# Kernel optimization log

Measured on AMD Instinct MI355X. Metric: run time of the kernel, lower is better.

## Reference

```python
import jax, jax.numpy as jnp
import numpy as np

H = 768        # bert hidden_size
HID = 512      # lstm_hidden
HALF = HID // 2
T = 20         # tagset_size
START, STOP = 18, 19
S = 16386      # input positions incl. CLS/SEP
NEG = -10000.0


def setup_inputs() -> dict:
    key = jax.random.key(0)
    ks = jax.random.split(key, 12)
    sc_x = 1.0
    x = jax.random.normal(ks[0], (1, S, H), dtype=jnp.float32)
    # PyTorch LSTM params (gate order i,f,g,o), one layer, bidirectional
    s_ih = 1.0 / np.sqrt(HALF)
    w_ih_f = jax.random.uniform(ks[1], (4 * HALF, H), jnp.float32, -s_ih, s_ih)
    w_hh_f = jax.random.uniform(ks[2], (4 * HALF, HALF), jnp.float32, -s_ih, s_ih)
    b_ih_f = jax.random.uniform(ks[3], (4 * HALF,), jnp.float32, -s_ih, s_ih)
    b_hh_f = jax.random.uniform(ks[4], (4 * HALF,), jnp.float32, -s_ih, s_ih)
    w_ih_b = jax.random.uniform(ks[5], (4 * HALF, H), jnp.float32, -s_ih, s_ih)
    w_hh_b = jax.random.uniform(ks[6], (4 * HALF, HALF), jnp.float32, -s_ih, s_ih)
    b_ih_b = jax.random.uniform(ks[7], (4 * HALF,), jnp.float32, -s_ih, s_ih)
    b_hh_b = jax.random.uniform(ks[8], (4 * HALF,), jnp.float32, -s_ih, s_ih)
    s_t = 1.0 / np.sqrt(HID)
    w_tag = jax.random.uniform(ks[9], (T, HID), jnp.float32, -s_t, s_t)
    b_tag = jax.random.uniform(ks[10], (T,), jnp.float32, -s_t, s_t)
    transitions = jax.random.normal(ks[11], (T, T), dtype=jnp.float32)
    transitions = transitions.at[START, :].set(NEG).at[:, STOP].set(NEG)
    return {
        "x": x,
        "w_ih_f": w_ih_f, "w_hh_f": w_hh_f, "b_ih_f": b_ih_f, "b_hh_f": b_hh_f,
        "w_ih_b": w_ih_b, "w_hh_b": w_hh_b, "b_ih_b": b_ih_b, "b_hh_b": b_hh_b,
        "w_tag": w_tag, "b_tag": b_tag, "transitions": transitions,
    }


def _lstm_one_step(xt, w_ih, b_ih, b_hh):
    # Original passes [1, N, H] to a batch_first=False LSTM => seq_len=1,
    # batch=N, zero initial state. So each token does ONE cell step:
    # h0=c0=0 => hh contribution is only b_hh.
    g = xt @ w_ih.T + b_ih + b_hh          # [N, 4*HALF]
    i, f, gg, o = jnp.split(g, 4, axis=-1)  # PyTorch gate order i,f,g,o
    c = jax.nn.sigmoid(i) * jnp.tanh(gg)    # f*c0 = 0
    return jax.nn.sigmoid(o) * jnp.tanh(c)  # [N, HALF]


def reference(x, w_ih_f, w_hh_f, b_ih_f, b_hh_f,
              w_ih_b, w_hh_b, b_ih_b, b_hh_b,
              w_tag, b_tag, transitions):
    tok = x[0, 1:-1, :]                     # narrow(1,1,S-2): drop CLS/SEP -> [N,H]
    h_f = _lstm_one_step(tok, w_ih_f, b_ih_f, b_hh_f)
    h_b = _lstm_one_step(tok, w_ih_b, b_ih_b, b_hh_b)
    enc = jnp.concatenate([h_f, h_b], axis=-1)   # [N, HID]
    feats = enc @ w_tag.T + b_tag                # [N, T] emission scores

    # ---- Viterbi decode (sequential DP over tokens) ----
    init = jnp.full((T,), NEG, dtype=feats.dtype).at[START].set(0.0)

    def vstep(fv, feat):
        scores = fv[None, :] + transitions       # [next_tag, prev_tag]
        bp = jnp.argmax(scores, axis=1)          # backpointers [T]
        fv_new = jnp.max(scores, axis=1) + feat
        return fv_new, bp

    fv, bps = jax.lax.scan(vstep, init, feats)   # bps: [N, T]
    terminal = fv + transitions[STOP]
    best = jnp.argmax(terminal)
    path_score = terminal[best]

    def btrack(b, bp):
        return bp[b], b                          # emit tag at time t, move to t-1

    _, best_path = jax.lax.scan(btrack, best, bps, reverse=True)  # [N] in time order
    return path_score, best_path
```

## Files before the change

### kernel.cpp

```cpp
#include <hip/hip_runtime.h>
#include <math.h>

#define HDIM 768
#define HIDD 512
#define NTOK 16384
#define NT 20
#define CHUNKS 128
#define CLEN 128

typedef unsigned short ushort_t;
typedef __attribute__((ext_vector_type(8))) short bf16x8;
typedef __attribute__((ext_vector_type(4))) float f32x4;

__device__ __forceinline__ float sigm(float x){ return 1.0f/(1.0f+expf(-x)); }

__device__ __forceinline__ ushort_t f2bf(float f){
    unsigned int u = __float_as_uint(f);
    unsigned int r = (u + 0x7fffu + ((u >> 16) & 1u)) >> 16;
    return (ushort_t)r;
}
__device__ __forceinline__ float bf2f(ushort_t b){
    return __uint_as_float(((unsigned int)b) << 16);
}

#define GLD16(gp, lp) __builtin_amdgcn_global_load_lds( \
    (const __attribute__((address_space(1))) void*)(gp), \
    (__attribute__((address_space(3))) void*)(lp), 16, 0, 0)

union U8 { ushort_t u[8]; uint4 v; };

__global__ __launch_bounds__(256) void conv_kernel(
    const float* __restrict__ wf, const float* __restrict__ wb,
    ushort_t* __restrict__ Bh, ushort_t* __restrict__ Bl)
{
    int t = blockIdx.x*256 + threadIdx.x;
    int n = t / 192, c4 = (t - n*192)*4;
    int dir = n / 768, nr = n - dir*768;
    int gate = nr >> 8, j = nr & 255;
    int wrow = j + ((gate==0)?0:((gate==1)?512:768));
    const float* src = dir ? wb : wf;
    const float4 v = *(const float4*)(src + (size_t)wrow*HDIM + c4);
    float f[4] = {v.x, v.y, v.z, v.w};
    ushort_t h[4], l[4];
    #pragma unroll
    for (int i=0;i<4;++i){
        h[i] = f2bf(f[i]);
        l[i] = f2bf(f[i] - bf2f(h[i]));
    }
    *(ushort4*)(Bh + (size_t)n*HDIM + c4) = make_ushort4(h[0],h[1],h[2],h[3]);
    *(ushort4*)(Bl + (size_t)n*HDIM + c4) = make_ushort4(l[0],l[1],l[2],l[3]);
}

__global__ __launch_bounds__(256, 2) void gemm_fused(
    const float* __restrict__ x,
    const ushort_t* __restrict__ Bh, const ushort_t* __restrict__ Bl,
    const float* __restrict__ bihf, const float* __restrict__ bhhf,
    const float* __restrict__ bihb, const float* __restrict__ bhhb,
    const float* __restrict__ wtag, float* __restrict__ featsp)
{
    __shared__ __align__(16) char smem[40960];
    ushort_t* As_h = (ushort_t*)smem;
    ushort_t* As_l = (ushort_t*)(smem + 4096);
    float* hbuf = (float*)smem;
    float* wts  = (float*)(smem + 16512);

    const int tid = threadIdx.x;
    const int bx = blockIdx.x;
    const int xcd = bx & 7, bidx = bx >> 3;
    const int q = bidx & 3, mt = (bidx >> 2)*8 + xcd;
    const int dir = q >> 1, j0 = (q & 1)*128;
    const int row0 = mt*64;
    const float* __restrict__ bih = dir ? bihb : bihf;
    const float* __restrict__ bhh = dir ? bhhb : bhhf;

    const int lane = tid & 63, wv = tid >> 6;
    const int wm = wv >> 1, wn = wv & 1;
    const int lm = lane & 15, lq = lane >> 4;
    const int wb8 = (tid & 192) * 8;

    const int P_ = tid >> 3, s_ = tid & 7;
    const int q_ = s_ ^ (P_ & 7);
    const int mA = (P_ << 1) | (q_ >> 2);
    const int k8s = q_ & 3;
    const int nB  = mA;
    const float* aSrc = x + (size_t)(row0 + mA + 1)*HDIM + k8s*8;
    const int bOff = nB*HDIM + k8s*8;

    int aoff[2], boff[4];
    #pragma unroll
    for (int f=0; f<2; ++f){
        int m = wm*32 + f*16 + lm;
        aoff[f] = ((m>>1)*8 + ((((m&1)<<2)|lq) ^ ((m>>1)&7)))*8;
    }
    #pragma unroll
    for (int f=0; f<4; ++f){
        int n = wn*64 + f*16 + lm;
        boff[f] = ((n>>1)*8 + ((((n&1)<<2)|lq) ^ ((n>>1)&7)))*8;
    }

    int jcol[4];
    #pragma unroll
    for (int fn=0; fn<4; ++fn) jcol[fn] = j0 + wn*64 + fn*16 + lm;

    float held[2][4][4];
    f32x4 acc[2][4];
    uint4 rh, rl;

    {
        const size_t bb = (size_t)(dir*768 + j0)*HDIM;
        GLD16(Bh + bb + bOff,            smem + 8192  + wb8*2);
        GLD16(Bh + bb + bOff + 64*HDIM,  smem + 12288 + wb8*2);
        GLD16(Bl + bb + bOff,            smem + 16384 + wb8*2);
        GLD16(Bl + bb + bOff + 64*HDIM,  smem + 20480 + wb8*2);
        float4 ra0 = *(const float4*)(aSrc);
        float4 ra1 = *(const float4*)(aSrc + 4);
        float f[8] = {ra0.x,ra0.y,ra0.z,ra0.w,ra1.x,ra1.y,ra1.z,ra1.w};
        U8 h8, l8;
        #pragma unroll
        for (int i=0;i<8;++i){
            ushort_t h = f2bf(f[i]);
            h8.u[i] = h; l8.u[i] = f2bf(f[i] - bf2f(h));
        }
        rh = h8.v; rl = l8.v;
    }

    #pragma unroll 1
    for (int p=0; p<3; ++p){
        #pragma unroll
        for (int fm=0; fm<2; ++fm)
            #pragma unroll
            for (int fn=0; fn<4; ++fn)
                acc[fm][fn] = (f32x4){0.f,0.f,0.f,0.f};

        #pragma unroll 1
        for (int kt=0; kt<24; ++kt){
            __syncthreads();
            *(uint4*)&As_h[tid*8] = rh;
            *(uint4*)&As_l[tid*8] = rl;
            __syncthreads();

            int nkt = kt + 1, np = p;
            if (nkt == 24){ nkt = 0; ++np; }
            if (np < 3){
                const int k0n = nkt*32;
                const size_t bb = (size_t)(dir*768 + np*256 + j0)*HDIM + k0n;
                char* bh_d = smem + 8192 + (nkt&1)*16384;
                GLD16(Bh + bb + bOff,           bh_d + wb8*2);
                GLD16(Bh + bb + bOff + 64*HDIM, bh_d + 4096 + wb8*2);
                GLD16(Bl + bb + bOff,           bh_d + 8192 + wb8*2);
                GLD16(Bl + bb + bOff + 64*HDIM, bh_d + 12288 + wb8*2);
                float4 ra0 = *(const float4*)(aSrc + k0n);
                float4 ra1 = *(const float4*)(aSrc + k0n + 4);
                float f[8] = {ra0.x,ra0.y,ra0.z,ra0.w,ra1.x,ra1.y,ra1.z,ra1.w};
                U8 h8, l8;
                #pragma unroll
                for (int i=0;i<8;++i){
                    ushort_t h = f2bf(f[i]);
                    h8.u[i] = h; l8.u[i] = f2bf(f[i] - bf2f(h));
                }
                rh = h8.v; rl = l8.v;
            }

            const ushort_t* Bsh = (const ushort_t*)(smem + 8192 + (kt&1)*16384);
            const ushort_t* Bsl = (const ushort_t*)(smem + 16384 + (kt&1)*16384);
            bf16x8 afh[2], afl[2];
            #pragma unroll
            for (int f=0; f<2; ++f){
                afh[f] = *(const bf16x8*)&As_h[aoff[f]];
                afl[f] = *(const bf16x8*)&As_l[aoff[f]];
            }
            #pragma unroll
            for (int fn=0; fn<4; ++fn){
                bf16x8 bh = *(const bf16x8*)&Bsh[boff[fn]];
                bf16x8 bl = *(const bf16x8*)&Bsl[boff[fn]];
                #pragma unroll
                for (int fm=0; fm<2; ++fm){
                    acc[fm][fn] = __builtin_amdgcn_mfma_f32_16x16x32_bf16(
                        afh[fm], bh, acc[fm][fn], 0, 0, 0);
                    acc[fm][fn] = __builtin_amdgcn_mfma_f32_16x16x32_bf16(
                        afl[fm], bh, acc[fm][fn], 0, 0, 0);
                    acc[fm][fn] = __builtin_amdgcn_mfma_f32_16x16x32_bf16(
                        afh[fm], bl, acc[fm][fn], 0, 0, 0);
                }
            }
        }

        const int gbase = (p==0) ? 0 : ((p==1) ? 512 : 768);
        float bias[4];
        #pragma unroll
        for (int fn=0; fn<4; ++fn)
            bias[fn] = bih[gbase + jcol[fn]] + bhh[gbase + jcol[fn]];

        if (p==0){
            #pragma unroll
            for (int fm=0; fm<2; ++fm)
                #pragma unroll
                for (int fn=0; fn<4; ++fn)
                    #pragma unroll
                    for (int r=0; r<4; ++r)
                        held[fm][fn][r] = sigm(acc[fm][fn][r] + bias[fn]);
        } else if (p==1){
            #pragma unroll
            for (int fm=0; fm<2; ++fm)
                #pragma unroll
                for (int fn=0; fn<4; ++fn)
                    #pragma unroll
                    for (int r=0; r<4; ++r)
                        held[fm][fn][r] *= tanhf(acc[fm][fn][r] + bias[fn]);
        } else {
            float hv[2][4][4];
            #pragma unroll
            for (int fm=0; fm<2; ++fm)
                #pragma unroll
                for (int fn=0; fn<4; ++fn)
                    #pragma unroll
                    for (int r=0; r<4; ++r)
                        hv[fm][fn][r] = sigm(acc[fm][fn][r] + bias[fn]) * tanhf(held[fm][fn][r]);

            __syncthreads();
            for (int i2=tid; i2<NT*128; i2+=256){
                int t = i2 >> 7, j = i2 & 127;
                wts[i2] = wtag[t*HIDD + dir*256 + j0 + j];
            }
            float* fq = featsp + (size_t)q * (NTOK*NT);
            #pragma unroll 1
            for (int ph=0; ph<2; ++ph){
                __syncthreads();
                if (wm == ph){
                    #pragma unroll
                    for (int fm=0; fm<2; ++fm)
                        #pragma unroll
                        for (int fn=0; fn<4; ++fn)
                            #pragma unroll
                            for (int r=0; r<4; ++r){
                                int mloc = fm*16 + lq*4 + r;
                                int jloc = wn*64 + fn*16 + lm;
                                hbuf[mloc*129 + jloc] = hv[fm][fn][r];
                            }
                }
                __syncthreads();
                const int mrow = tid & 31, grp = tid >> 5;
                if (grp < 5){
                    const int tg0 = grp*4;
                    float s[4] = {0.f,0.f,0.f,0.f};
                    for (int j=0;j<128;++j){
                        float h = hbuf[mrow*129 + j];
                        #pragma unroll
                        for (int tt=0; tt<4; ++tt)
                            s[tt] = fmaf(h, wts[(tg0+tt)*128 + j], s[tt]);
                    }
                    const int mglob = row0 + ph*32 + mrow;
                    #pragma unroll
                    for (int tt=0; tt<4; ++tt)
                        fq[(size_t)mglob*NT + tg0 + tt] = s[tt];
                }
            }
        }
    }
}

__device__ __forceinline__ void load_fl(
    const float* __restrict__ featsp, const float* __restrict__ btg,
    float* fl, int c, int tid, int nthr)
{
    const float4* p0 = (const float4*)(featsp);
    const float4* p1 = (const float4*)(featsp + (size_t)NTOK*NT);
    const float4* p2 = (const float4*)(featsp + (size_t)2*NTOK*NT);
    const float4* p3 = (const float4*)(featsp + (size_t)3*NTOK*NT);
    const int base = c*(CLEN*NT/4);
    for (int idx=tid; idx<CLEN*NT/4; idx+=nthr){
        float4 a = p0[base+idx], b = p1[base+idx];
        float4 d = p2[base+idx], e = p3[base+idx];
        float4 v;
        v.x = (a.x+b.x)+(d.x+e.x);
        v.y = (a.y+b.y)+(d.y+e.y);
        v.z = (a.z+b.z)+(d.z+e.z);
        v.w = (a.w+b.w)+(d.w+e.w);
        int t0 = (idx*4) % 20;
        v.x += btg[t0]; v.y += btg[t0+1]; v.z += btg[t0+2]; v.w += btg[t0+3];
        ((float4*)fl)[idx] = v;
    }
}

__global__ __launch_bounds__(512) void vit_chunkmat(
    const float* __restrict__ featsp, const float* __restrict__ btag,
    const float* __restrict__ trans, float* __restrict__ Pall)
{
    __shared__ float fl[CLEN*NT];
    __shared__ float Pb[2][NT*NT];
    const int c = blockIdx.x, tid = threadIdx.x;
    load_fl(featsp, btag, fl, c, tid, 512);
    const bool act = tid < NT*NT;
    const int i = tid/20, j = tid - i*20;
    float tr[NT];
    if (act){
        #pragma unroll
        for (int k=0;k<NT;++k) tr[k] = trans[i*NT+k];
        Pb[0][tid] = (i==j) ? 0.f : -1e30f;
    }
    __syncthreads();
    int cur = 0;
    for (int t=0;t<CLEN;++t){
        float m = -3.0e38f;
        if (act){
            #pragma unroll
            for (int k=0;k<NT;++k) m = fmaxf(m, tr[k] + Pb[cur][k*NT+j]);
            m += fl[t*NT+i];
            Pb[cur^1][tid] = m;
        }
        __syncthreads();
        cur ^= 1;
    }
    if (act) Pall[(size_t)c*(NT*NT) + tid] = Pb[cur][tid];
}

__global__ __launch_bounds__(128) void vit_scan(
    const float* __restrict__ Pall, const float* __restrict__ trans,
    float* __restrict__ fvstart, float* __restrict__ dout, int* __restrict__ bestws)
{
    __shared__ float Pb[NT*NT];
    __shared__ float fv[NT];
    const int tid = threadIdx.x;
    float4 pn = {0.f,0.f,0.f,0.f};
    if (tid<100) pn = ((const float4*)Pall)[tid];
    if (tid<NT) fv[tid] = (tid==18) ? 0.f : -10000.f;
    for (int c=0;c<CHUNKS;++c){
        if (tid<100) ((float4*)Pb)[tid] = pn;
        if (tid<100 && c+1<CHUNKS) pn = ((const float4*)(Pall + (size_t)(c+1)*(NT*NT)))[tid];
        __syncthreads();
        if (tid<NT) fvstart[c*NT+tid] = fv[tid];
        float nf = -3.0e38f;
        if (tid<NT){
            #pragma unroll
            for (int j=0;j<NT;++j) nf = fmaxf(nf, Pb[tid*NT+j] + fv[j]);
        }
        __syncthreads();
        if (tid<NT) fv[tid] = nf;
    }
    __syncthreads();
    if (tid==0){
        float best = -3.0e38f; int bidx = 0;
        for (int j=0;j<NT;++j){
            float tv = fv[j] + trans[19*NT+j];
            if (tv > best){ best = tv; bidx = j; }
        }
        dout[0] = best;
        bestws[0] = bidx;
    }
}

__global__ __launch_bounds__(64) void vit_replay(
    const float* __restrict__ featsp, const float* __restrict__ btag,
    const float* __restrict__ trans, const float* __restrict__ fvstart,
    unsigned int* __restrict__ bpout, int* __restrict__ Hout)
{
    __shared__ float fl[CLEN*NT];
    __shared__ float fv[NT];
    __shared__ unsigned char bp[CLEN*NT];
    const int c = blockIdx.x, tid = threadIdx.x;
    load_fl(featsp, btag, fl, c, tid, 64);
    float tr[NT];
    if (tid<NT){
        fv[tid] = fvstart[c*NT+tid];
        #pragma unroll
        for (int k=0;k<NT;++k) tr[k] = trans[tid*NT+k];
    }
    __syncthreads();
    for (int t=0;t<CLEN;++t){
        float best = 0.f; int bj = 0;
        if (tid<NT){
            best = tr[0] + fv[0];
            #pragma unroll
            for (int j=1;j<NT;++j){
                float v = tr[j] + fv[j];
                if (v > best){ best = v; bj = j; }
            }
        }
        __syncthreads();
        if (tid<NT){
            fv[tid] = best + fl[t*NT+tid];
            bp[t*NT+tid] = (unsigned char)bj;
        }
        __syncthreads();
    }
    for (int idx=tid; idx<CLEN*NT/4; idx+=64)
        bpout[(size_t)c*(CLEN*NT/4) + idx] = ((unsigned int*)bp)[idx];
    if (tid<NT){
        int m = tid;
        for (int t=CLEN-1;t>=0;--t) m = bp[t*NT+m];
        Hout[c*NT+tid] = m;
    }
}

__global__ __launch_bounds__(64) void bt_fill(
    const unsigned int* __restrict__ bpin, const int* __restrict__ Hin,
    const int* __restrict__ bestws, float* __restrict__ dout)
{
    __shared__ int Hl[CHUNKS*NT];
    __shared__ unsigned char bp[CLEN*NT];
    __shared__ float ob[CLEN];
    const int c = blockIdx.x, tid = threadIdx.x;
    for (int idx=tid; idx<CHUNKS*NT; idx+=64) Hl[idx] = Hin[idx];
    for (int idx=tid; idx<CLEN*NT/4; idx+=64)
        ((unsigned int*)bp)[idx] = bpin[(size_t)c*(CLEN*NT/4) + idx];
    __syncthreads();
    if (tid==0){
        int e = bestws[0];
        for (int cc=CHUNKS-1; cc>c; --cc) e = Hl[cc*NT+e];
        for (int t=CLEN-1;t>=0;--t){ ob[t] = (float)e; e = bp[t*NT+e]; }
    }
    __syncthreads();
    for (int idx=tid; idx<CLEN; idx+=64)
        dout[1 + c*CLEN + idx] = ob[idx];
}

extern "C" void kernel_launch(void* const* d_in, const int* in_sizes, int n_in,
                              void* d_out, int out_size, void* d_ws, size_t ws_size,
                              hipStream_t stream)
{
    const float* x    = (const float*)d_in[0];
    const float* wf   = (const float*)d_in[1];
    const float* bihf = (const float*)d_in[3];
    const float* bhhf = (const float*)d_in[4];
    const float* wb   = (const float*)d_in[5];
    const float* bihb = (const float*)d_in[7];
    const float* bhhb = (const float*)d_in[8];
    const float* wtag = (const float*)d_in[9];
    const float* btag = (const float*)d_in[10];
    const float* trans= (const float*)d_in[11];
    float* out = (float*)d_out;

    char* w = (char*)d_ws;
    ushort_t* Bh = (ushort_t*)w;         w += 2359296;
    ushort_t* Bl = (ushort_t*)w;         w += 2359296;
    float* featsp = (float*)w;           w += 5242880;
    float* Pall  = (float*)w;            w += 204800;
    float* fvst  = (float*)w;            w += 10240;
    int* Hmap    = (int*)w;              w += 10240;
    unsigned int* bp = (unsigned int*)w; w += 327680;
    int* best    = (int*)w;

    conv_kernel<<<1152, 256, 0, stream>>>(wf, wb, Bh, Bl);
    gemm_fused<<<1024, 256, 0, stream>>>(x, Bh, Bl, bihf, bhhf, bihb, bhhb,
                                         wtag, featsp);
    vit_chunkmat<<<CHUNKS, 512, 0, stream>>>(featsp, btag, trans, Pall);
    vit_scan<<<1, 128, 0, stream>>>(Pall, trans, fvst, out, best);
    vit_replay<<<CHUNKS, 64, 0, stream>>>(featsp, btag, trans, fvst, bp, Hmap);
    bt_fill<<<CHUNKS, 64, 0, stream>>>(bp, Hmap, best, out);
}
```

Before: 432.6 us.

## Compute all three gates per tile in one K pass and fold scan into replay

Each GEMM block now accumulates the i, g and o gate tiles together over a single K sweep, using narrower 64-column tiles and twice as many blocks, and the three B tiles are double-buffered in larger shared memory. This reuses each A tile across all gates, so x is no longer reloaded and re-split into bf16 three times. The price is eight partial emission buffers instead of four, which doubles featsp traffic, plus higher LDS use that may lower occupancy. The serial vit_scan kernel is removed: each replay block recomputes its own chunk start by applying all earlier chunk max-plus matrices, which saves a launch but adds redundant work in the later blocks.

```diff
diff --git a/kernel.cpp b/kernel.cpp
--- a/kernel.cpp
+++ b/kernel.cpp
@@ -58,17 +58,17 @@
     const float* __restrict__ bihb, const float* __restrict__ bhhb,
     const float* __restrict__ wtag, float* __restrict__ featsp)
 {
-    __shared__ __align__(16) char smem[40960];
+    __shared__ __align__(16) char smem[57344];
     ushort_t* As_h = (ushort_t*)smem;
     ushort_t* As_l = (ushort_t*)(smem + 4096);
     float* hbuf = (float*)smem;
-    float* wts  = (float*)(smem + 16512);
+    float* wts  = (float*)(smem + 8448);
 
     const int tid = threadIdx.x;
     const int bx = blockIdx.x;
     const int xcd = bx & 7, bidx = bx >> 3;
-    const int q = bidx & 3, mt = (bidx >> 2)*8 + xcd;
-    const int dir = q >> 1, j0 = (q & 1)*128;
+    const int q = bidx & 7, mt = (bidx >> 3)*8 + xcd;
+    const int dir = q >> 2, j0 = (q & 3)*64;
     const int row0 = mt*64;
     const float* __restrict__ bih = dir ? bihb : bihf;
     const float* __restrict__ bhh = dir ? bhhb : bhhf;
@@ -76,42 +76,49 @@
     const int lane = tid & 63, wv = tid >> 6;
     const int wm = wv >> 1, wn = wv & 1;
     const int lm = lane & 15, lq = lane >> 4;
-    const int wb8 = (tid & 192) * 8;
+    const int wbB = (tid & 192) * 16;
 
     const int P_ = tid >> 3, s_ = tid & 7;
     const int q_ = s_ ^ (P_ & 7);
     const int mA = (P_ << 1) | (q_ >> 2);
     const int k8s = q_ & 3;
-    const int nB  = mA;
     const float* aSrc = x + (size_t)(row0 + mA + 1)*HDIM + k8s*8;
-    const int bOff = nB*HDIM + k8s*8;
-
-    int aoff[2], boff[4];
+    size_t bOff[3];
+    #pragma unroll
+    for (int g=0; g<3; ++g)
+        bOff[g] = (size_t)(dir*768 + g*256 + j0 + mA)*HDIM + k8s*8;
+
+    int aoffB[2], boffB[2];
     #pragma unroll
     for (int f=0; f<2; ++f){
         int m = wm*32 + f*16 + lm;
-        aoff[f] = ((m>>1)*8 + ((((m&1)<<2)|lq) ^ ((m>>1)&7)))*8;
-    }
-    #pragma unroll
-    for (int f=0; f<4; ++f){
-        int n = wn*64 + f*16 + lm;
-        boff[f] = ((n>>1)*8 + ((((n&1)<<2)|lq) ^ ((n>>1)&7)))*8;
-    }
-
-    int jcol[4];
-    #pragma unroll
-    for (int fn=0; fn<4; ++fn) jcol[fn] = j0 + wn*64 + fn*16 + lm;
-
-    float held[2][4][4];
-    f32x4 acc[2][4];
+        aoffB[f] = ((m>>1)*8 + ((((m&1)<<2)|lq) ^ ((m>>1)&7)))*16;
+        int n = wn*32 + f*16 + lm;
+        boffB[f] = ((n>>1)*8 + ((((n&1)<<2)|lq) ^ ((n>>1)&7)))*16;
+    }
+
+    int jcol[2];
+    #pragma unroll
+    for (int f=0; f<2; ++f) jcol[f] = j0 + wn*32 + f*16 + lm;
+
+    f32x4 acc[3][2][2];
+    #pragma unroll
+    for (int g=0; g<3; ++g)
+        #pragma unroll
+        for (int fm=0; fm<2; ++fm)
+            #pragma unroll
+            for (int fn=0; fn<2; ++fn)
+                acc[g][fm][fn] = (f32x4){0.f,0.f,0.f,0.f};
+
     uint4 rh, rl;
 
     {
-        const size_t bb = (size_t)(dir*768 + j0)*HDIM;
-        GLD16(Bh + bb + bOff,            smem + 8192  + wb8*2);
-        GLD16(Bh + bb + bOff + 64*HDIM,  smem + 12288 + wb8*2);
-        GLD16(Bl + bb + bOff,            smem + 16384 + wb8*2);
-        GLD16(Bl + bb + bOff + 64*HDIM,  smem + 20480 + wb8*2);
+        char* bb = smem + 8192;
+        #pragma unroll
+        for (int g=0; g<3; ++g){
+            GLD16(Bh + bOff[g], bb + g*8192 + wbB);
+            GLD16(Bl + bOff[g], bb + g*8192 + 4096 + wbB);
+        }
         float4 ra0 = *(const float4*)(aSrc);
         float4 ra1 = *(const float4*)(aSrc + 4);
         float f[8] = {ra0.x,ra0.y,ra0.z,ra0.w,ra1.x,ra1.y,ra1.z,ra1.w};
@@ -125,136 +132,114 @@
     }
 
     #pragma unroll 1
-    for (int p=0; p<3; ++p){
-        #pragma unroll
-        for (int fm=0; fm<2; ++fm)
-            #pragma unroll
-            for (int fn=0; fn<4; ++fn)
-                acc[fm][fn] = (f32x4){0.f,0.f,0.f,0.f};
-
-        #pragma unroll 1
-        for (int kt=0; kt<24; ++kt){
-            __syncthreads();
-            *(uint4*)&As_h[tid*8] = rh;
-            *(uint4*)&As_l[tid*8] = rl;
-            __syncthreads();
-
-            int nkt = kt + 1, np = p;
-            if (nkt == 24){ nkt = 0; ++np; }
-            if (np < 3){
-                const int k0n = nkt*32;
-                const size_t bb = (size_t)(dir*768 + np*256 + j0)*HDIM + k0n;
-                char* bh_d = smem + 8192 + (nkt&1)*16384;
-                GLD16(Bh + bb + bOff,           bh_d + wb8*2);
-                GLD16(Bh + bb + bOff + 64*HDIM, bh_d + 4096 + wb8*2);
-                GLD16(Bl + bb + bOff,           bh_d + 8192 + wb8*2);
-                GLD16(Bl + bb + bOff + 64*HDIM, bh_d + 12288 + wb8*2);
-                float4 ra0 = *(const float4*)(aSrc + k0n);
-                float4 ra1 = *(const float4*)(aSrc + k0n + 4);
-                float f[8] = {ra0.x,ra0.y,ra0.z,ra0.w,ra1.x,ra1.y,ra1.z,ra1.w};
-                U8 h8, l8;
-                #pragma unroll
-                for (int i=0;i<8;++i){
-                    ushort_t h = f2bf(f[i]);
-                    h8.u[i] = h; l8.u[i] = f2bf(f[i] - bf2f(h));
-                }
-                rh = h8.v; rl = l8.v;
-            }
-
-            const ushort_t* Bsh = (const ushort_t*)(smem + 8192 + (kt&1)*16384);
-            const ushort_t* Bsl = (const ushort_t*)(smem + 16384 + (kt&1)*16384);
-            bf16x8 afh[2], afl[2];
-            #pragma unroll
-            for (int f=0; f<2; ++f){
-                afh[f] = *(const bf16x8*)&As_h[aoff[f]];
-                afl[f] = *(const bf16x8*)&As_l[aoff[f]];
-            }
-            #pragma unroll
-            for (int fn=0; fn<4; ++fn){
-                bf16x8 bh = *(const bf16x8*)&Bsh[boff[fn]];
-                bf16x8 bl = *(const bf16x8*)&Bsl[boff[fn]];
+    for (int kt=0; kt<24; ++kt){
+        __syncthreads();
+        *(uint4*)&As_h[tid*8] = rh;
+        *(uint4*)&As_l[tid*8] = rl;
+        __syncthreads();
+
+        if (kt < 23){
+            const int k0n = (kt+1)*32;
+            char* bb = smem + 8192 + ((kt+1)&1)*24576;
+            #pragma unroll
+            for (int g=0; g<3; ++g){
+                GLD16(Bh + bOff[g] + k0n, bb + g*8192 + wbB);
+                GLD16(Bl + bOff[g] + k0n, bb + g*8192 + 4096 + wbB);
+            }
+            float4 ra0 = *(const float4*)(aSrc + k0n);
+            float4 ra1 = *(const float4*)(aSrc + k0n + 4);
+            float f[8] = {ra0.x,ra0.y,ra0.z,ra0.w,ra1.x,ra1.y,ra1.z,ra1.w};
+            U8 h8, l8;
+            #pragma unroll
+            for (int i=0;i<8;++i){
+                ushort_t h = f2bf(f[i]);
+                h8.u[i] = h; l8.u[i] = f2bf(f[i] - bf2f(h));
+            }
+            rh = h8.v; rl = l8.v;
+        }
+
+        const char* bb = smem + 8192 + (kt&1)*24576;
+        bf16x8 afh[2], afl[2];
+        #pragma unroll
+        for (int f=0; f<2; ++f){
+            afh[f] = *(const bf16x8*)(smem + aoffB[f]);
+            afl[f] = *(const bf16x8*)(smem + 4096 + aoffB[f]);
+        }
+        #pragma unroll
+        for (int g=0; g<3; ++g){
+            const char* bg = bb + g*8192;
+            #pragma unroll
+            for (int fn=0; fn<2; ++fn){
+                bf16x8 bh = *(const bf16x8*)(bg + boffB[fn]);
+                bf16x8 bl = *(const bf16x8*)(bg + 4096 + boffB[fn]);
                 #pragma unroll
                 for (int fm=0; fm<2; ++fm){
-                    acc[fm][fn] = __builtin_amdgcn_mfma_f32_16x16x32_bf16(
-                        afh[fm], bh, acc[fm][fn], 0, 0, 0);
-                    acc[fm][fn] = __builtin_amdgcn_mfma_f32_16x16x32_bf16(
-                        afl[fm], bh, acc[fm][fn], 0, 0, 0);
-                    acc[fm][fn] = __builtin_amdgcn_mfma_f32_16x16x32_bf16(
-                        afh[fm], bl, acc[fm][fn], 0, 0, 0);
+                    acc[g][fm][fn] = __builtin_amdgcn_mfma_f32_16x16x32_bf16(
+                        afh[fm], bh, acc[g][fm][fn], 0, 0, 0);
+                    acc[g][fm][fn] = __builtin_amdgcn_mfma_f32_16x16x32_bf16(
+                        afl[fm], bh, acc[g][fm][fn], 0, 0, 0);
+                    acc[g][fm][fn] = __builtin_amdgcn_mfma_f32_16x16x32_bf16(
+                        afh[fm], bl, acc[g][fm][fn], 0, 0, 0);
                 }
             }
         }
-
-        const int gbase = (p==0) ? 0 : ((p==1) ? 512 : 768);
-        float bias[4];
-        #pragma unroll
-        for (int fn=0; fn<4; ++fn)
-            bias[fn] = bih[gbase + jcol[fn]] + bhh[gbase + jcol[fn]];
-
-        if (p==0){
+    }
+
+    float bi[2], bg_[2], bo[2];
+    #pragma unroll
+    for (int f=0; f<2; ++f){
+        bi[f]  = bih[jcol[f]]       + bhh[jcol[f]];
+        bg_[f] = bih[512 + jcol[f]] + bhh[512 + jcol[f]];
+        bo[f]  = bih[768 + jcol[f]] + bhh[768 + jcol[f]];
+    }
+    float hv[2][2][4];
+    #pragma unroll
+    for (int fm=0; fm<2; ++fm)
+        #pragma unroll
+        for (int fn=0; fn<2; ++fn)
+            #pragma unroll
+            for (int r=0; r<4; ++r){
+                float cv = sigm(acc[0][fm][fn][r] + bi[fn]) *
+                           tanhf(acc[1][fm][fn][r] + bg_[fn]);
+                hv[fm][fn][r] = sigm(acc[2][fm][fn][r] + bo[fn]) * tanhf(cv);
+            }
+
+    __syncthreads();
+    for (int i2=tid; i2<NT*64; i2+=256){
+        int t = i2 >> 6, j = i2 & 63;
+        wts[i2] = wtag[t*HIDD + dir*256 + j0 + j];
+    }
+    float* fq = featsp + (size_t)q * (NTOK*NT);
+    #pragma unroll 1
+    for (int ph=0; ph<2; ++ph){
+        __syncthreads();
+        if (wm == ph){
             #pragma unroll
             for (int fm=0; fm<2; ++fm)
                 #pragma unroll
-                for (int fn=0; fn<4; ++fn)
+                for (int fn=0; fn<2; ++fn)
                     #pragma unroll
-                    for (int r=0; r<4; ++r)
-                        held[fm][fn][r] = sigm(acc[fm][fn][r] + bias[fn]);
-        } else if (p==1){
-            #pragma unroll
-            for (int fm=0; fm<2; ++fm)
+                    for (int r=0; r<4; ++r){
+                        int mloc = fm*16 + lq*4 + r;
+                        int jloc = wn*32 + fn*16 + lm;
+                        hbuf[mloc*65 + jloc] = hv[fm][fn][r];
+                    }
+        }
+        __syncthreads();
+        const int mrow = tid & 31, grp = tid >> 5;
+        if (grp < 5){
+            const int tg0 = grp*4;
+            float s[4] = {0.f,0.f,0.f,0.f};
+            for (int j=0;j<64;++j){
+                float h = hbuf[mrow*65 + j];
                 #pragma unroll
-                for (int fn=0; fn<4; ++fn)
-                    #pragma unroll
-                    for (int r=0; r<4; ++r)
-                        held[fm][fn][r] *= tanhf(acc[fm][fn][r] + bias[fn]);
-        } else {
-            float hv[2][4][4];
-            #pragma unroll
-            for (int fm=0; fm<2; ++fm)
-                #pragma unroll
-                for (int fn=0; fn<4; ++fn)
-                    #pragma unroll
-                    for (int r=0; r<4; ++r)
-                        hv[fm][fn][r] = sigm(acc[fm][fn][r] + bias[fn]) * tanhf(held[fm][fn][r]);
-
-            __syncthreads();
-            for (int i2=tid; i2<NT*128; i2+=256){
-                int t = i2 >> 7, j = i2 & 127;
-                wts[i2] = wtag[t*HIDD + dir*256 + j0 + j];
-            }
-            float* fq = featsp + (size_t)q * (NTOK*NT);
-            #pragma unroll 1
-            for (int ph=0; ph<2; ++ph){
-                __syncthreads();
-                if (wm == ph){
-                    #pragma unroll
-                    for (int fm=0; fm<2; ++fm)
-                        #pragma unroll
-                        for (int fn=0; fn<4; ++fn)
-                            #pragma unroll
-                            for (int r=0; r<4; ++r){
-                                int mloc = fm*16 + lq*4 + r;
-                                int jloc = wn*64 + fn*16 + lm;
-                                hbuf[mloc*129 + jloc] = hv[fm][fn][r];
-                            }
-                }
-                __syncthreads();
-                const int mrow = tid & 31, grp = tid >> 5;
-                if (grp < 5){
-                    const int tg0 = grp*4;
-                    float s[4] = {0.f,0.f,0.f,0.f};
-                    for (int j=0;j<128;++j){
-                        float h = hbuf[mrow*129 + j];
-                        #pragma unroll
-                        for (int tt=0; tt<4; ++tt)
-                            s[tt] = fmaf(h, wts[(tg0+tt)*128 + j], s[tt]);
-                    }
-                    const int mglob = row0 + ph*32 + mrow;
-                    #pragma unroll
-                    for (int tt=0; tt<4; ++tt)
-                        fq[(size_t)mglob*NT + tg0 + tt] = s[tt];
-                }
-            }
+                for (int tt=0; tt<4; ++tt)
+                    s[tt] = fmaf(h, wts[(tg0+tt)*64 + j], s[tt]);
+            }
+            const int mglob = row0 + ph*32 + mrow;
+            #pragma unroll
+            for (int tt=0; tt<4; ++tt)
+                fq[(size_t)mglob*NT + tg0 + tt] = s[tt];
         }
     }
 }
@@ -263,19 +248,17 @@
     const float* __restrict__ featsp, const float* __restrict__ btg,
     float* fl, int c, int tid, int nthr)
 {
-    const float4* p0 = (const float4*)(featsp);
-    const float4* p1 = (const float4*)(featsp + (size_t)NTOK*NT);
-    const float4* p2 = (const float4*)(featsp + (size_t)2*NTOK*NT);
-    const float4* p3 = (const float4*)(featsp + (size_t)3*NTOK*NT);
     const int base = c*(CLEN*NT/4);
     for (int idx=tid; idx<CLEN*NT/4; idx+=nthr){
-        float4 a = p0[base+idx], b = p1[base+idx];
-        float4 d = p2[base+idx], e = p3[base+idx];
+        float4 s[8];
+        #pragma unroll
+        for (int p=0; p<8; ++p)
+            s[p] = ((const float4*)(featsp + (size_t)p*NTOK*NT))[base+idx];
         float4 v;
-        v.x = (a.x+b.x)+(d.x+e.x);
-        v.y = (a.y+b.y)+(d.y+e.y);
-        v.z = (a.z+b.z)+(d.z+e.z);
-        v.w = (a.w+b.w)+(d.w+e.w);
+        v.x = ((s[0].x+s[1].x)+(s[2].x+s[3].x)) + ((s[4].x+s[5].x)+(s[6].x+s[7].x));
+        v.y = ((s[0].y+s[1].y)+(s[2].y+s[3].y)) + ((s[4].y+s[5].y)+(s[6].y+s[7].y));
+        v.z = ((s[0].z+s[1].z)+(s[2].z+s[3].z)) + ((s[4].z+s[5].z)+(s[6].z+s[7].z));
+        v.w = ((s[0].w+s[1].w)+(s[2].w+s[3].w)) + ((s[4].w+s[5].w)+(s[6].w+s[7].w));
         int t0 = (idx*4) % 20;
         v.x += btg[t0]; v.y += btg[t0+1]; v.z += btg[t0+2]; v.w += btg[t0+3];
         ((float4*)fl)[idx] = v;
@@ -314,21 +297,26 @@
     if (act) Pall[(size_t)c*(NT*NT) + tid] = Pb[cur][tid];
 }
 
-__global__ __launch_bounds__(128) void vit_scan(
-    const float* __restrict__ Pall, const float* __restrict__ trans,
-    float* __restrict__ fvstart, float* __restrict__ dout, int* __restrict__ bestws)
-{
+__global__ __launch_bounds__(128) void vit_replay(
+    const float* __restrict__ featsp, const float* __restrict__ btag,
+    const float* __restrict__ trans, const float* __restrict__ Pall,
+    unsigned int* __restrict__ bpout, int* __restrict__ Hout,
+    float* __restrict__ dout, int* __restrict__ bestws)
+{
+    __shared__ float fl[CLEN*NT];
+    __shared__ float fv[NT];
     __shared__ float Pb[NT*NT];
-    __shared__ float fv[NT];
-    const int tid = threadIdx.x;
+    __shared__ unsigned char bp[CLEN*NT];
+    const int c = blockIdx.x, tid = threadIdx.x;
+    load_fl(featsp, btag, fl, c, tid, 128);
+    if (tid<NT) fv[tid] = (tid==18) ? 0.f : -10000.f;
     float4 pn = {0.f,0.f,0.f,0.f};
-    if (tid<100) pn = ((const float4*)Pall)[tid];
-    if (tid<NT) fv[tid] = (tid==18) ? 0.f : -10000.f;
-    for (int c=0;c<CHUNKS;++c){
+    if (tid<100 && c>0) pn = ((const float4*)Pall)[tid];
+    __syncthreads();
+    for (int cc=0; cc<c; ++cc){
         if (tid<100) ((float4*)Pb)[tid] = pn;
-        if (tid<100 && c+1<CHUNKS) pn = ((const float4*)(Pall + (size_t)(c+1)*(NT*NT)))[tid];
-        __syncthreads();
-        if (tid<NT) fvstart[c*NT+tid] = fv[tid];
+        if (tid<100 && cc+1<c) pn = ((const float4*)(Pall + (size_t)(cc+1)*(NT*NT)))[tid];
+        __syncthreads();
         float nf = -3.0e38f;
         if (tid<NT){
             #pragma unroll
@@ -336,32 +324,10 @@
         }
         __syncthreads();
         if (tid<NT) fv[tid] = nf;
-    }
-    __syncthreads();
-    if (tid==0){
-        float best = -3.0e38f; int bidx = 0;
-        for (int j=0;j<NT;++j){
-            float tv = fv[j] + trans[19*NT+j];
-            if (tv > best){ best = tv; bidx = j; }
-        }
-        dout[0] = best;
-        bestws[0] = bidx;
-    }
-}
-
-__global__ __launch_bounds__(64) void vit_replay(
-    const float* __restrict__ featsp, const float* __restrict__ btag,
-    const float* __restrict__ trans, const float* __restrict__ fvstart,
-    unsigned int* __restrict__ bpout, int* __restrict__ Hout)
-{
-    __shared__ float fl[CLEN*NT];
-    __shared__ float fv[NT];
-    __shared__ unsigned char bp[CLEN*NT];
-    const int c = blockIdx.x, tid = threadIdx.x;
-    load_fl(featsp, btag, fl, c, tid, 64);
+        __syncthreads();
+    }
     float tr[NT];
     if (tid<NT){
-        fv[tid] = fvstart[c*NT+tid];
         #pragma unroll
         for (int k=0;k<NT;++k) tr[k] = trans[tid*NT+k];
     }
@@ -383,12 +349,21 @@
         }
         __syncthreads();
     }
-    for (int idx=tid; idx<CLEN*NT/4; idx+=64)
+    for (int idx=tid; idx<CLEN*NT/4; idx+=128)
         bpout[(size_t)c*(CLEN*NT/4) + idx] = ((unsigned int*)bp)[idx];
     if (tid<NT){
         int m = tid;
         for (int t=CLEN-1;t>=0;--t) m = bp[t*NT+m];
         Hout[c*NT+tid] = m;
+    }
+    if (c == CHUNKS-1 && tid == 0){
+        float best = -3.0e38f; int bidx = 0;
+        for (int j=0;j<NT;++j){
+            float tv = fv[j] + trans[19*NT+j];
+            if (tv > best){ best = tv; bidx = j; }
+        }
+        dout[0] = best;
+        bestws[0] = bidx;
     }
 }
 
@@ -433,18 +408,17 @@
     char* w = (char*)d_ws;
     ushort_t* Bh = (ushort_t*)w;         w += 2359296;
     ushort_t* Bl = (ushort_t*)w;         w += 2359296;
-    float* featsp = (float*)w;           w += 5242880;
+    float* featsp = (float*)w;           w += 10485760;
     float* Pall  = (float*)w;            w += 204800;
-    float* fvst  = (float*)w;            w += 10240;
     int* Hmap    = (int*)w;              w += 10240;
     unsigned int* bp = (unsigned int*)w; w += 327680;
     int* best    = (int*)w;
 
     conv_kernel<<<1152, 256, 0, stream>>>(wf, wb, Bh, Bl);
-    gemm_fused<<<1024, 256, 0, stream>>>(x, Bh, Bl, bihf, bhhf, bihb, bhhb,
+    gemm_fused<<<2048, 256, 0, stream>>>(x, Bh, Bl, bihf, bhhf, bihb, bhhb,
                                          wtag, featsp);
     vit_chunkmat<<<CHUNKS, 512, 0, stream>>>(featsp, btag, trans, Pall);
-    vit_scan<<<1, 128, 0, stream>>>(Pall, trans, fvst, out, best);
-    vit_replay<<<CHUNKS, 64, 0, stream>>>(featsp, btag, trans, fvst, bp, Hmap);
+    vit_replay<<<CHUNKS, 128, 0, stream>>>(featsp, btag, trans, Pall, bp, Hmap,
+                                           out, best);
     bt_fill<<<CHUNKS, 64, 0, stream>>>(bp, Hmap, best, out);
 }
```

Result: faster. 393.9 us (-8.9%).
